# Performance work log

Measured on AMD Instinct MI355X. Metric: run time of the kernel, lower is better.

Reference implementation:

```python
import jax, jax.numpy as jnp
import numpy as np

D_MODEL, D_INNER, D_STATE, DT_RANK, D_CONV = 768, 1536, 16, 48, 4
B, L = 2, 2048


def setup_inputs() -> dict:
    key = jax.random.key(0)
    ks = jax.random.split(key, 8)
    s = 0.02
    return {
        "x": jax.random.normal(ks[0], (B, L, D_MODEL), jnp.float32),
        "norm_w": jnp.ones((D_MODEL,), jnp.float32),
        "in_proj_w": jax.random.normal(ks[1], (2 * D_INNER, D_MODEL), jnp.float32) * s,
        "conv_w": jax.random.normal(ks[2], (D_INNER, 1, D_CONV), jnp.float32) * s,
        "conv_b": jnp.zeros((D_INNER,), jnp.float32),
        "x_proj_w": jax.random.normal(ks[3], (DT_RANK + 2 * D_STATE, D_INNER), jnp.float32) * s,
        "dt_proj_w": jax.random.normal(ks[4], (D_INNER, DT_RANK), jnp.float32) * s,
        "dt_proj_b": jax.random.normal(ks[5], (D_INNER,), jnp.float32) * s,
        "A_log": jnp.broadcast_to(jnp.log(jnp.arange(1, D_STATE + 1, dtype=jnp.float32)), (D_INNER, D_STATE)).copy(),
        "D": jnp.ones((D_INNER,), jnp.float32),
        "out_proj_w": jax.random.normal(ks[6], (D_MODEL, D_INNER), jnp.float32) * s,
    }


def _mamba_block(x, norm_w, in_proj_w, conv_w, conv_b, x_proj_w,
                 dt_proj_w, dt_proj_b, A_log, D, out_proj_w):
    residual = x
    # RMSNorm
    h = x * jax.lax.rsqrt(jnp.mean(x * x, axis=-1, keepdims=True) + 1e-5) * norm_w
    # in_proj -> chunk into (hs, gate)
    xz = jnp.einsum('bld,ed->ble', h, in_proj_w)          # [B,L,2*Di]
    xh, z = jnp.split(xz, 2, axis=-1)                     # each [B,L,Di]
    # causal depthwise conv1d (kernel D_CONV) + SiLU
    xt = jnp.transpose(xh, (0, 2, 1))                     # [B,Di,L]
    xt = jnp.pad(xt, ((0, 0), (0, 0), (D_CONV - 1, 0)))
    xc = jax.lax.conv_general_dilated(xt, conv_w, (1,), 'VALID',
                                      feature_group_count=D_INNER)
    xc = jax.nn.silu(xc + conv_b[None, :, None])
    xc = jnp.transpose(xc, (0, 2, 1))                     # [B,L,Di]
    # x_proj -> (dt, B, C)
    proj = jnp.einsum('bld,ed->ble', xc, x_proj_w)        # [B,L,dt_rank+2N]
    dt, Bm, Cm = jnp.split(proj, [DT_RANK, DT_RANK + D_STATE], axis=-1)
    delta = jax.nn.softplus(jnp.einsum('blr,dr->bld', dt, dt_proj_w) + dt_proj_b)  # [B,L,Di]
    A = -jnp.exp(A_log)                                   # [Di,N]
    dA = jnp.exp(delta[..., None] * A)                    # [B,L,Di,N]
    dBx = delta[..., None] * Bm[:, :, None, :] * xc[..., None]  # [B,L,Di,N]
    # selective scan over the sequence axis
    def step(hst, inp):
        dA_t, dBx_t, C_t = inp                            # [B,Di,N],[B,Di,N],[B,N]
        hst = dA_t * hst + dBx_t
        y = jnp.einsum('bdn,bn->bd', hst, C_t)
        return hst, y
    h0 = jnp.zeros((x.shape[0], D_INNER, D_STATE), x.dtype)
    _, ys = jax.lax.scan(step, h0, (jnp.moveaxis(dA, 1, 0),
                                    jnp.moveaxis(dBx, 1, 0),
                                    jnp.moveaxis(Cm, 1, 0)))
    y = jnp.moveaxis(ys, 0, 1)                            # [B,L,Di]
    y = y + xc * D                                        # skip connection D
    y = y * jax.nn.silu(z)                                # gate
    out = jnp.einsum('bld,ed->ble', y, out_proj_w)        # [B,L,Dm]
    return residual + out, residual


def reference(x, norm_w, in_proj_w, conv_w, conv_b, x_proj_w,
              dt_proj_w, dt_proj_b, A_log, D, out_proj_w):
    return _mamba_block(x, norm_w, in_proj_w, conv_w, conv_b, x_proj_w,
                        dt_proj_w, dt_proj_b, A_log, D, out_proj_w)
```

## Files before the change

kernel.cpp:

```cpp
#include <hip/hip_runtime.h>
#include <cstdint>
#include <cstddef>

typedef __bf16 bf16_t;
typedef __bf16 bf16x8 __attribute__((ext_vector_type(8)));
typedef float  f32x4  __attribute__((ext_vector_type(4)));

#define D_MODEL 768
#define D_INNER 1536
#define D_STATE 16
#define DT_RANK 48
#define NB      2
#define SEQ     2048
#define NTOK    (NB*SEQ)
#define XPROJ_N (DT_RANK + 2*D_STATE)
#define LC      32
#define NCHUNK  (SEQ/LC)

typedef __attribute__((address_space(1))) void gvoid_t;
typedef __attribute__((address_space(3))) void lvoid_t;
__device__ __forceinline__ void g2lds16(const bf16_t* g, bf16_t* l) {
    __builtin_amdgcn_global_load_lds((gvoid_t*)g, (lvoid_t*)l, 16, 0, 0);
}

__global__ __launch_bounds__(256)
void cvt4_kernel(const float* __restrict__ s0, bf16_t* __restrict__ d0, int n0,
                 const float* __restrict__ s1, bf16_t* __restrict__ d1, int n1,
                 const float* __restrict__ s2, bf16_t* __restrict__ d2, int n2,
                 const float* __restrict__ s3, bf16_t* __restrict__ d3, int n3) {
    int i = blockIdx.x * 256 + threadIdx.x;
    if (i < n0) { d0[i] = (bf16_t)s0[i]; return; }
    i -= n0;
    if (i < n1) { d1[i] = (bf16_t)s1[i]; return; }
    i -= n1;
    if (i < n2) { d2[i] = (bf16_t)s2[i]; return; }
    i -= n2;
    if (i < n3) { d3[i] = (bf16_t)s3[i]; }
}

__global__ __launch_bounds__(256)
void rmsnorm_kernel(const float* __restrict__ x, const float* __restrict__ w,
                    bf16_t* __restrict__ h) {
    int t = blockIdx.x;
    int tid = threadIdx.x;
    const float* xr = x + (size_t)t * D_MODEL;
    float v[3];
    float ss = 0.f;
#pragma unroll
    for (int i = 0; i < 3; i++) { v[i] = xr[tid + 256*i]; ss += v[i]*v[i]; }
#pragma unroll
    for (int off = 32; off >= 1; off >>= 1) ss += __shfl_down(ss, off);
    __shared__ float red[4];
    int lane = tid & 63, wv = tid >> 6;
    if (lane == 0) red[wv] = ss;
    __syncthreads();
    float tot = red[0] + red[1] + red[2] + red[3];
    float r = rsqrtf(tot * (1.f/(float)D_MODEL) + 1e-5f);
#pragma unroll
    for (int i = 0; i < 3; i++)
        h[(size_t)t*D_MODEL + tid + 256*i] = (bf16_t)(v[i] * r * w[tid + 256*i]);
}

template<int MODE>
__global__ __launch_bounds__(256)
void gemm_nt128(const bf16_t* __restrict__ A, int lda,
                const bf16_t* __restrict__ B, int ldb,
                void* __restrict__ Cv, int ldc, int K,
                const float* __restrict__ resid, float* __restrict__ resid_out) {
    __shared__ __align__(16) bf16_t As[128*32];
    __shared__ __align__(16) bf16_t Bs[128*32];
    const int tid = threadIdx.x;
    const int wave = tid >> 6, lane = tid & 63;
    const int quad = lane >> 4, l16 = lane & 15;
    const int m0 = blockIdx.x * 128, n0 = blockIdx.y * 128;
    const int wr = (wave >> 1) * 64, wc = (wave & 1) * 64;

    const int s0 = tid, s1 = tid + 256;
    const int r0 = s0 >> 2, q0 = ((s0 & 3) ^ ((r0 >> 1) & 3)) << 3;
    const int r1 = s1 >> 2, q1 = ((s1 & 3) ^ ((r1 >> 1) & 3)) << 3;

    f32x4 acc[4][4] = {};

    for (int k0 = 0; k0 < K; k0 += 32) {
        g2lds16(A + (size_t)(m0 + r0)*lda + k0 + q0, &As[wave*512]);
        g2lds16(A + (size_t)(m0 + r1)*lda + k0 + q1, &As[wave*512 + 2048]);
        g2lds16(B + (size_t)(n0 + r0)*ldb + k0 + q0, &Bs[wave*512]);
        g2lds16(B + (size_t)(n0 + r1)*ldb + k0 + q1, &Bs[wave*512 + 2048]);
        __syncthreads();

        bf16x8 af[4], bfr[4];
#pragma unroll
        for (int i = 0; i < 4; i++) {
            int rr = wr + i*16 + l16;
            af[i] = *(const bf16x8*)&As[rr*32 + ((quad ^ ((rr >> 1) & 3)) << 3)];
        }
#pragma unroll
        for (int j = 0; j < 4; j++) {
            int rr = wc + j*16 + l16;
            bfr[j] = *(const bf16x8*)&Bs[rr*32 + ((quad ^ ((rr >> 1) & 3)) << 3)];
        }
#pragma unroll
        for (int i = 0; i < 4; i++)
#pragma unroll
            for (int j = 0; j < 4; j++)
                acc[i][j] = __builtin_amdgcn_mfma_f32_16x16x32_bf16(af[i], bfr[j], acc[i][j], 0, 0, 0);
        __syncthreads();
    }

#pragma unroll
    for (int i = 0; i < 4; i++) {
#pragma unroll
        for (int j = 0; j < 4; j++) {
            int n = n0 + wc + j*16 + l16;
#pragma unroll
            for (int rr = 0; rr < 4; rr++) {
                int m = m0 + wr + i*16 + quad*4 + rr;
                size_t idx = (size_t)m * ldc + n;
                float v = acc[i][j][rr];
                if (MODE == 2) {
                    float rx = resid[idx];
                    ((float*)Cv)[idx] = v + rx;
                    resid_out[idx] = rx;
                } else {
                    ((bf16_t*)Cv)[idx] = (bf16_t)v;
                }
            }
        }
    }
}

template<int MODE>
__global__ __launch_bounds__(256)
void gemm_nt(const bf16_t* __restrict__ A, int lda,
             const bf16_t* __restrict__ B, int ldb,
             void* __restrict__ Cv, int ldc, int N, int K,
             const float* __restrict__ bias) {
    __shared__ __align__(16) bf16_t As[64*32];
    __shared__ __align__(16) bf16_t Bs[64*32];
    const int tid = threadIdx.x;
    const int m0 = blockIdx.x * 64, n0 = blockIdx.y * 64;
    const int r  = tid >> 2, p8 = (tid & 3) << 3;
    const int q8 = (((tid & 3) ^ ((r >> 1) & 3)) << 3);
    const int wave = tid >> 6, lane = tid & 63;
    const int quad = lane >> 4, l16 = lane & 15;

    f32x4 acc[4] = {{0.f,0.f,0.f,0.f},{0.f,0.f,0.f,0.f},
                    {0.f,0.f,0.f,0.f},{0.f,0.f,0.f,0.f}};

    for (int k0 = 0; k0 < K; k0 += 32) {
        int gk = k0 + q8;
        uint4 va = {0u,0u,0u,0u};
        if (gk + 8 <= K)
            va = *(const uint4*)(A + (size_t)(m0 + r) * lda + gk);
        *(uint4*)&As[r*32 + p8] = va;

        uint4 vb = {0u,0u,0u,0u};
        int nr = n0 + r;
        if (nr < N && gk + 8 <= K)
            vb = *(const uint4*)(B + (size_t)nr * ldb + gk);
        *(uint4*)&Bs[r*32 + p8] = vb;

        __syncthreads();
        int ra = wave*16 + l16;
        bf16x8 af = *(const bf16x8*)&As[ra*32 + ((quad ^ ((ra >> 1) & 3)) << 3)];
#pragma unroll
        for (int nt = 0; nt < 4; nt++) {
            int rb = nt*16 + l16;
            bf16x8 bfg = *(const bf16x8*)&Bs[rb*32 + ((quad ^ ((rb >> 1) & 3)) << 3)];
            acc[nt] = __builtin_amdgcn_mfma_f32_16x16x32_bf16(af, bfg, acc[nt], 0, 0, 0);
        }
        __syncthreads();
    }

#pragma unroll
    for (int nt = 0; nt < 4; nt++) {
        int n = n0 + nt*16 + l16;
        if (n >= N) continue;
#pragma unroll
        for (int rr = 0; rr < 4; rr++) {
            int m = m0 + wave*16 + quad*4 + rr;
            float v = acc[nt][rr];
            size_t idx = (size_t)m * ldc + n;
            if (MODE == 1) {
                float u = v + bias[n];
                float sp = (u > 20.f) ? u : log1pf(__expf(u));
                ((bf16_t*)Cv)[idx] = (bf16_t)sp;
            } else {
                ((bf16_t*)Cv)[idx] = (bf16_t)v;
            }
        }
    }
}

__global__ __launch_bounds__(256)
void conv_silu_kernel(const bf16_t* __restrict__ xz,
                      const float* __restrict__ cw,
                      const float* __restrict__ cb,
                      bf16_t* __restrict__ xc) {
    int t = blockIdx.x;
    int l = t & (SEQ - 1);
    for (int d = threadIdx.x; d < D_INNER; d += 256) {
        float acc = cb[d];
#pragma unroll
        for (int k = 0; k < 4; k++) {
            int ll = l - 3 + k;
            if (ll >= 0)
                acc += (float)xz[(size_t)(t - 3 + k) * (2*D_INNER) + d] * cw[d*4 + k];
        }
        float s = acc / (1.f + __expf(-acc));
        xc[(size_t)t * D_INNER + d] = (bf16_t)s;
    }
}

__global__ __launch_bounds__(256)
void scan_part1(const bf16_t* __restrict__ delta,
                const bf16_t* __restrict__ xc,
                const bf16_t* __restrict__ proj,
                const float* __restrict__ A_log,
                float* __restrict__ chunk_h, float* __restrict__ chunk_P) {
    const int tid = threadIdx.x;
    const int d = blockIdx.x * 256 + tid;
    const int c = blockIdx.y;
    const int b = blockIdx.z;
    __shared__ float Bs[LC][D_STATE];
    for (int i = tid; i < LC*D_STATE; i += 256) {
        int l = i >> 4, n = i & 15;
        size_t t = (size_t)b*SEQ + (size_t)c*LC + l;
        Bs[l][n] = (float)proj[t*XPROJ_N + DT_RANK + n];
    }
    __syncthreads();
    float Av2[D_STATE];
#pragma unroll
    for (int n = 0; n < D_STATE; n++)
        Av2[n] = -__expf(A_log[d*D_STATE + n]) * 1.44269504f;
    float s[D_STATE], P[D_STATE];
#pragma unroll
    for (int n = 0; n < D_STATE; n++) { s[n] = 0.f; P[n] = 1.f; }
    const size_t tbase = (size_t)b*SEQ + (size_t)c*LC;
    for (int l = 0; l < LC; l++) {
        size_t t = tbase + l;
        float dv  = (float)delta[t*D_INNER + d];
        float xcv = (float)xc[t*D_INNER + d];
        float dx = dv * xcv;
#pragma unroll
        for (int n = 0; n < D_STATE; n++) {
            float a = __builtin_amdgcn_exp2f(dv * Av2[n]);
            s[n] = a * s[n] + dx * Bs[l][n];
            P[n] *= a;
        }
    }
    size_t base = (((size_t)b*NCHUNK + c)*D_INNER + d)*D_STATE;
#pragma unroll
    for (int n = 0; n < D_STATE; n++) {
        chunk_h[base + n] = s[n];
        chunk_P[base + n] = P[n];
    }
}

__global__ __launch_bounds__(256)
void scan_part2(float* __restrict__ chunk_h, const float* __restrict__ chunk_P) {
    int gid = blockIdx.x * 256 + threadIdx.x;
    int b  = gid / (D_INNER * D_STATE);
    int dn = gid - b * (D_INNER * D_STATE);
    float H = 0.f;
    for (int c = 0; c < NCHUNK; c++) {
        size_t idx = ((size_t)b*NCHUNK + c)*D_INNER*D_STATE + dn;
        float S = chunk_h[idx];
        float P = chunk_P[idx];
        chunk_h[idx] = H;
        H = P * H + S;
    }
}

__global__ __launch_bounds__(256)
void scan_part3(const bf16_t* __restrict__ delta,
                const bf16_t* __restrict__ xc,
                const bf16_t* __restrict__ proj,
                const bf16_t* __restrict__ xz,
                const float* __restrict__ A_log,
                const float* __restrict__ Dw,
                const float* __restrict__ chunk_h,
                bf16_t* __restrict__ y) {
    const int tid = threadIdx.x;
    const int d = blockIdx.x * 256 + tid;
    const int c = blockIdx.y;
    const int b = blockIdx.z;
    __shared__ float Bs[LC][D_STATE];
    __shared__ float Cs[LC][D_STATE];
    for (int i = tid; i < LC*D_STATE; i += 256) {
        int l = i >> 4, n = i & 15;
        size_t t = (size_t)b*SEQ + (size_t)c*LC + l;
        Bs[l][n] = (float)proj[t*XPROJ_N + DT_RANK + n];
        Cs[l][n] = (float)proj[t*XPROJ_N + DT_RANK + D_STATE + n];
    }
    __syncthreads();
    float Av2[D_STATE];
#pragma unroll
    for (int n = 0; n < D_STATE; n++)
        Av2[n] = -__expf(A_log[d*D_STATE + n]) * 1.44269504f;
    const float Dv = Dw[d];
    float s[D_STATE];
    size_t base = (((size_t)b*NCHUNK + c)*D_INNER + d)*D_STATE;
#pragma unroll
    for (int n = 0; n < D_STATE; n++) s[n] = chunk_h[base + n];
    const size_t tbase = (size_t)b*SEQ + (size_t)c*LC;
    for (int l = 0; l < LC; l++) {
        size_t t = tbase + l;
        float dv  = (float)delta[t*D_INNER + d];
        float xcv = (float)xc[t*D_INNER + d];
        float dx = dv * xcv;
        float acc = 0.f;
#pragma unroll
        for (int n = 0; n < D_STATE; n++) {
            float a = __builtin_amdgcn_exp2f(dv * Av2[n]);
            s[n] = a * s[n] + dx * Bs[l][n];
            acc += s[n] * Cs[l][n];
        }
        float zf = (float)xz[t*(2*D_INNER) + D_INNER + d];
        float g = zf / (1.f + __expf(-zf));
        y[t*D_INNER + d] = (bf16_t)((acc + xcv * Dv) * g);
    }
}

extern "C" void kernel_launch(void* const* d_in, const int* in_sizes, int n_in,
                              void* d_out, int out_size, void* d_ws, size_t ws_size,
                              hipStream_t stream) {
    const float* x          = (const float*)d_in[0];
    const float* norm_w     = (const float*)d_in[1];
    const float* in_proj_w  = (const float*)d_in[2];
    const float* conv_w     = (const float*)d_in[3];
    const float* conv_b     = (const float*)d_in[4];
    const float* x_proj_w   = (const float*)d_in[5];
    const float* dt_proj_w  = (const float*)d_in[6];
    const float* dt_proj_b  = (const float*)d_in[7];
    const float* A_log      = (const float*)d_in[8];
    const float* Dw         = (const float*)d_in[9];
    const float* out_proj_w = (const float*)d_in[10];

    float* out0 = (float*)d_out;
    float* out1 = out0 + (size_t)NTOK * D_MODEL;

    const int n_inw = 2*D_INNER*D_MODEL;
    const int n_xpw = XPROJ_N*D_INNER;
    const int n_dtw = D_INNER*DT_RANK;
    const int n_opw = D_MODEL*D_INNER;
    const size_t n_chunkst = (size_t)NB*NCHUNK*D_INNER*D_STATE;

    char* ws = (char*)d_ws;
    bf16_t* w_in  = (bf16_t*)ws;  ws += (size_t)n_inw * sizeof(bf16_t);
    bf16_t* w_xp  = (bf16_t*)ws;  ws += (size_t)n_xpw * sizeof(bf16_t);
    bf16_t* w_dt  = (bf16_t*)ws;  ws += (size_t)n_dtw * sizeof(bf16_t);
    bf16_t* w_op  = (bf16_t*)ws;  ws += (size_t)n_opw * sizeof(bf16_t);
    bf16_t* h     = (bf16_t*)ws;  ws += (size_t)NTOK * D_MODEL   * sizeof(bf16_t);
    bf16_t* xz    = (bf16_t*)ws;  ws += (size_t)NTOK * 2*D_INNER * sizeof(bf16_t);
    bf16_t* xc    = (bf16_t*)ws;  ws += (size_t)NTOK * D_INNER   * sizeof(bf16_t);
    bf16_t* proj  = (bf16_t*)ws;  ws += (size_t)NTOK * XPROJ_N   * sizeof(bf16_t);
    bf16_t* delta = (bf16_t*)ws;  ws += (size_t)NTOK * D_INNER   * sizeof(bf16_t);
    bf16_t* y     = (bf16_t*)ws;  ws += (size_t)NTOK * D_INNER   * sizeof(bf16_t);
    float*  ch    = (float*)ws;   ws += n_chunkst * sizeof(float);
    float*  cP    = (float*)ws;   ws += n_chunkst * sizeof(float);

    const int n_cvt = n_inw + n_xpw + n_dtw + n_opw;
    cvt4_kernel<<<(n_cvt+255)/256, 256, 0, stream>>>(
        in_proj_w, w_in, n_inw, x_proj_w, w_xp, n_xpw,
        dt_proj_w, w_dt, n_dtw, out_proj_w, w_op, n_opw);

    rmsnorm_kernel<<<NTOK, 256, 0, stream>>>(x, norm_w, h);
    gemm_nt128<0><<<dim3(NTOK/128, (2*D_INNER)/128), 256, 0, stream>>>(
        h, D_MODEL, w_in, D_MODEL, xz, 2*D_INNER, D_MODEL, nullptr, nullptr);
    conv_silu_kernel<<<NTOK, 256, 0, stream>>>(xz, conv_w, conv_b, xc);
    gemm_nt<0><<<dim3(NTOK/64, 2), 256, 0, stream>>>(
        xc, D_INNER, w_xp, D_INNER, proj, XPROJ_N, XPROJ_N, D_INNER, nullptr);
    gemm_nt<1><<<dim3(NTOK/64, D_INNER/64), 256, 0, stream>>>(
        proj, XPROJ_N, w_dt, DT_RANK, delta, D_INNER, D_INNER, DT_RANK, dt_proj_b);
    scan_part1<<<dim3(D_INNER/256, NCHUNK, NB), 256, 0, stream>>>(
        delta, xc, proj, A_log, ch, cP);
    scan_part2<<<(int)((size_t)NB*D_INNER*D_STATE/256), 256, 0, stream>>>(ch, cP);
    scan_part3<<<dim3(D_INNER/256, NCHUNK, NB), 256, 0, stream>>>(
        delta, xc, proj, xz, A_log, Dw, ch, y);
    gemm_nt128<2><<<dim3(NTOK/128, D_MODEL/128), 256, 0, stream>>>(
        y, D_INNER, w_op, D_INNER, out0, D_MODEL, D_INNER, x, out1);
}
```

Before: 319.1 us.

## Double-buffer LDS in 128-tile GEMM and route dt_proj through it with padded K

Rewrites the 128x128 GEMM main loop to prefetch the next K-slice into a second LDS buffer while computing on the current one. This drops one barrier per iteration so global-to-LDS loads can overlap the MFMA work. The dt_proj GEMM, which applies softplus to the bias-added result, moves from the 64-tile kernel onto the 128-tile kernel. For that, the dt weight is zero-padded from rank 48 to 64 and the extra columns of proj are read against zero weights. The trade-offs are double the LDS per block, which may lower occupancy, and a small amount of wasted multiply work on the padding.

```diff
diff --git a/kernel.cpp b/kernel.cpp
--- a/kernel.cpp
+++ b/kernel.cpp
@@ -10,6 +10,7 @@
 #define D_INNER 1536
 #define D_STATE 16
 #define DT_RANK 48
+#define DT_K    64
 #define NB      2
 #define SEQ     2048
 #define NTOK    (NB*SEQ)
@@ -24,18 +25,23 @@
 }
 
 __global__ __launch_bounds__(256)
-void cvt4_kernel(const float* __restrict__ s0, bf16_t* __restrict__ d0, int n0,
+void cvt3_kernel(const float* __restrict__ s0, bf16_t* __restrict__ d0, int n0,
                  const float* __restrict__ s1, bf16_t* __restrict__ d1, int n1,
-                 const float* __restrict__ s2, bf16_t* __restrict__ d2, int n2,
-                 const float* __restrict__ s3, bf16_t* __restrict__ d3, int n3) {
+                 const float* __restrict__ s2, bf16_t* __restrict__ d2, int n2) {
     int i = blockIdx.x * 256 + threadIdx.x;
     if (i < n0) { d0[i] = (bf16_t)s0[i]; return; }
     i -= n0;
     if (i < n1) { d1[i] = (bf16_t)s1[i]; return; }
     i -= n1;
-    if (i < n2) { d2[i] = (bf16_t)s2[i]; return; }
-    i -= n2;
-    if (i < n3) { d3[i] = (bf16_t)s3[i]; }
+    if (i < n2) { d2[i] = (bf16_t)s2[i]; }
+}
+
+__global__ __launch_bounds__(256)
+void cvt_pad_dt_kernel(const float* __restrict__ src, bf16_t* __restrict__ dst) {
+    int i = blockIdx.x * 256 + threadIdx.x;
+    if (i >= D_INNER * DT_K) return;
+    int row = i >> 6, col = i & 63;
+    dst[i] = (col < DT_RANK) ? (bf16_t)src[row * DT_RANK + col] : (bf16_t)0.f;
 }
 
 __global__ __launch_bounds__(256)
@@ -66,9 +72,10 @@
 void gemm_nt128(const bf16_t* __restrict__ A, int lda,
                 const bf16_t* __restrict__ B, int ldb,
                 void* __restrict__ Cv, int ldc, int K,
+                const float* __restrict__ bias,
                 const float* __restrict__ resid, float* __restrict__ resid_out) {
-    __shared__ __align__(16) bf16_t As[128*32];
-    __shared__ __align__(16) bf16_t Bs[128*32];
+    __shared__ __align__(16) bf16_t As[2][128*32];
+    __shared__ __align__(16) bf16_t Bs[2][128*32];
     const int tid = threadIdx.x;
     const int wave = tid >> 6, lane = tid & 63;
     const int quad = lane >> 4, l16 = lane & 15;
@@ -79,32 +86,46 @@
     const int r0 = s0 >> 2, q0 = ((s0 & 3) ^ ((r0 >> 1) & 3)) << 3;
     const int r1 = s1 >> 2, q1 = ((s1 & 3) ^ ((r1 >> 1) & 3)) << 3;
 
+    const bf16_t* Ar0 = A + (size_t)(m0 + r0)*lda + q0;
+    const bf16_t* Ar1 = A + (size_t)(m0 + r1)*lda + q1;
+    const bf16_t* Br0 = B + (size_t)(n0 + r0)*ldb + q0;
+    const bf16_t* Br1 = B + (size_t)(n0 + r1)*ldb + q1;
+
     f32x4 acc[4][4] = {};
-
-    for (int k0 = 0; k0 < K; k0 += 32) {
-        g2lds16(A + (size_t)(m0 + r0)*lda + k0 + q0, &As[wave*512]);
-        g2lds16(A + (size_t)(m0 + r1)*lda + k0 + q1, &As[wave*512 + 2048]);
-        g2lds16(B + (size_t)(n0 + r0)*ldb + k0 + q0, &Bs[wave*512]);
-        g2lds16(B + (size_t)(n0 + r1)*ldb + k0 + q1, &Bs[wave*512 + 2048]);
+    const int nit = K >> 5;
+
+    g2lds16(Ar0, &As[0][wave*512]);
+    g2lds16(Ar1, &As[0][wave*512 + 2048]);
+    g2lds16(Br0, &Bs[0][wave*512]);
+    g2lds16(Br1, &Bs[0][wave*512 + 2048]);
+
+    for (int it = 0; it < nit; it++) {
         __syncthreads();
-
+        if (it + 1 < nit) {
+            int k = (it + 1) << 5;
+            int nb = (it + 1) & 1;
+            g2lds16(Ar0 + k, &As[nb][wave*512]);
+            g2lds16(Ar1 + k, &As[nb][wave*512 + 2048]);
+            g2lds16(Br0 + k, &Bs[nb][wave*512]);
+            g2lds16(Br1 + k, &Bs[nb][wave*512 + 2048]);
+        }
+        const int buf = it & 1;
         bf16x8 af[4], bfr[4];
 #pragma unroll
         for (int i = 0; i < 4; i++) {
             int rr = wr + i*16 + l16;
-            af[i] = *(const bf16x8*)&As[rr*32 + ((quad ^ ((rr >> 1) & 3)) << 3)];
+            af[i] = *(const bf16x8*)&As[buf][rr*32 + ((quad ^ ((rr >> 1) & 3)) << 3)];
         }
 #pragma unroll
         for (int j = 0; j < 4; j++) {
             int rr = wc + j*16 + l16;
-            bfr[j] = *(const bf16x8*)&Bs[rr*32 + ((quad ^ ((rr >> 1) & 3)) << 3)];
+            bfr[j] = *(const bf16x8*)&Bs[buf][rr*32 + ((quad ^ ((rr >> 1) & 3)) << 3)];
         }
 #pragma unroll
         for (int i = 0; i < 4; i++)
 #pragma unroll
             for (int j = 0; j < 4; j++)
                 acc[i][j] = __builtin_amdgcn_mfma_f32_16x16x32_bf16(af[i], bfr[j], acc[i][j], 0, 0, 0);
-        __syncthreads();
     }
 
 #pragma unroll
@@ -117,7 +138,11 @@
                 int m = m0 + wr + i*16 + quad*4 + rr;
                 size_t idx = (size_t)m * ldc + n;
                 float v = acc[i][j][rr];
-                if (MODE == 2) {
+                if (MODE == 1) {
+                    float u = v + bias[n];
+                    float sp = (u > 20.f) ? u : log1pf(__expf(u));
+                    ((bf16_t*)Cv)[idx] = (bf16_t)sp;
+                } else if (MODE == 2) {
                     float rx = resid[idx];
                     ((float*)Cv)[idx] = v + rx;
                     resid_out[idx] = rx;
@@ -129,12 +154,10 @@
     }
 }
 
-template<int MODE>
-__global__ __launch_bounds__(256)
-void gemm_nt(const bf16_t* __restrict__ A, int lda,
-             const bf16_t* __restrict__ B, int ldb,
-             void* __restrict__ Cv, int ldc, int N, int K,
-             const float* __restrict__ bias) {
+__global__ __launch_bounds__(256)
+void gemm_nt64(const bf16_t* __restrict__ A, int lda,
+               const bf16_t* __restrict__ B, int ldb,
+               bf16_t* __restrict__ C, int ldc, int N, int K) {
     __shared__ __align__(16) bf16_t As[64*32];
     __shared__ __align__(16) bf16_t Bs[64*32];
     const int tid = threadIdx.x;
@@ -149,14 +172,11 @@
 
     for (int k0 = 0; k0 < K; k0 += 32) {
         int gk = k0 + q8;
-        uint4 va = {0u,0u,0u,0u};
-        if (gk + 8 <= K)
-            va = *(const uint4*)(A + (size_t)(m0 + r) * lda + gk);
+        uint4 va = *(const uint4*)(A + (size_t)(m0 + r) * lda + gk);
         *(uint4*)&As[r*32 + p8] = va;
-
         uint4 vb = {0u,0u,0u,0u};
         int nr = n0 + r;
-        if (nr < N && gk + 8 <= K)
+        if (nr < N)
             vb = *(const uint4*)(B + (size_t)nr * ldb + gk);
         *(uint4*)&Bs[r*32 + p8] = vb;
 
@@ -179,15 +199,7 @@
 #pragma unroll
         for (int rr = 0; rr < 4; rr++) {
             int m = m0 + wave*16 + quad*4 + rr;
-            float v = acc[nt][rr];
-            size_t idx = (size_t)m * ldc + n;
-            if (MODE == 1) {
-                float u = v + bias[n];
-                float sp = (u > 20.f) ? u : log1pf(__expf(u));
-                ((bf16_t*)Cv)[idx] = (bf16_t)sp;
-            } else {
-                ((bf16_t*)Cv)[idx] = (bf16_t)v;
-            }
+            C[(size_t)m * ldc + n] = (bf16_t)acc[nt][rr];
         }
     }
 }
@@ -342,7 +354,7 @@
 
     const int n_inw = 2*D_INNER*D_MODEL;
     const int n_xpw = XPROJ_N*D_INNER;
-    const int n_dtw = D_INNER*DT_RANK;
+    const int n_dtw = D_INNER*DT_K;
     const int n_opw = D_MODEL*D_INNER;
     const size_t n_chunkst = (size_t)NB*NCHUNK*D_INNER*D_STATE;
 
@@ -360,24 +372,27 @@
     float*  ch    = (float*)ws;   ws += n_chunkst * sizeof(float);
     float*  cP    = (float*)ws;   ws += n_chunkst * sizeof(float);
 
-    const int n_cvt = n_inw + n_xpw + n_dtw + n_opw;
-    cvt4_kernel<<<(n_cvt+255)/256, 256, 0, stream>>>(
-        in_proj_w, w_in, n_inw, x_proj_w, w_xp, n_xpw,
-        dt_proj_w, w_dt, n_dtw, out_proj_w, w_op, n_opw);
+    const int n_cvt = n_inw + n_xpw + n_opw;
+    cvt3_kernel<<<(n_cvt+255)/256, 256, 0, stream>>>(
+        in_proj_w, w_in, n_inw, x_proj_w, w_xp, n_xpw, out_proj_w, w_op, n_opw);
+    cvt_pad_dt_kernel<<<(n_dtw+255)/256, 256, 0, stream>>>(dt_proj_w, w_dt);
 
     rmsnorm_kernel<<<NTOK, 256, 0, stream>>>(x, norm_w, h);
     gemm_nt128<0><<<dim3(NTOK/128, (2*D_INNER)/128), 256, 0, stream>>>(
-        h, D_MODEL, w_in, D_MODEL, xz, 2*D_INNER, D_MODEL, nullptr, nullptr);
+        h, D_MODEL, w_in, D_MODEL, xz, 2*D_INNER, D_MODEL,
+        nullptr, nullptr, nullptr);
     conv_silu_kernel<<<NTOK, 256, 0, stream>>>(xz, conv_w, conv_b, xc);
-    gemm_nt<0><<<dim3(NTOK/64, 2), 256, 0, stream>>>(
-        xc, D_INNER, w_xp, D_INNER, proj, XPROJ_N, XPROJ_N, D_INNER, nullptr);
-    gemm_nt<1><<<dim3(NTOK/64, D_INNER/64), 256, 0, stream>>>(
-        proj, XPROJ_N, w_dt, DT_RANK, delta, D_INNER, D_INNER, DT_RANK, dt_proj_b);
+    gemm_nt64<<<dim3(NTOK/64, 2), 256, 0, stream>>>(
+        xc, D_INNER, w_xp, D_INNER, proj, XPROJ_N, XPROJ_N, D_INNER);
+    gemm_nt128<1><<<dim3(NTOK/128, D_INNER/128), 256, 0, stream>>>(
+        proj, XPROJ_N, w_dt, DT_K, delta, D_INNER, DT_K,
+        dt_proj_b, nullptr, nullptr);
     scan_part1<<<dim3(D_INNER/256, NCHUNK, NB), 256, 0, stream>>>(
         delta, xc, proj, A_log, ch, cP);
     scan_part2<<<(int)((size_t)NB*D_INNER*D_STATE/256), 256, 0, stream>>>(ch, cP);
     scan_part3<<<dim3(D_INNER/256, NCHUNK, NB), 256, 0, stream>>>(
         delta, xc, proj, xz, A_log, Dw, ch, y);
     gemm_nt128<2><<<dim3(NTOK/128, D_MODEL/128), 256, 0, stream>>>(
-        y, D_INNER, w_op, D_INNER, out0, D_MODEL, D_INNER, x, out1);
-}
+        y, D_INNER, w_op, D_INNER, out0, D_MODEL, D_INNER,
+        nullptr, x, out1);
+}
```

After: 324.5 us. Within noise of the previous version (+1.7%).
